# Performance work log

Measured on AMD Instinct MI355X. Metric: run time of the kernel, lower is better.

Reference implementation:

```python
import jax, jax.numpy as jnp
import numpy as np

# ---- MMAL-Net canonical configuration (baked constants of the module) ----
STRIDE = 32          # backbone stride: feature cell -> input pixels
FM = 14              # feature-map side (448 / 32)
RATIOS = [[4, 4], [3, 5], [5, 3],
          [6, 6], [5, 7], [7, 5],
          [8, 8], [6, 10], [10, 6], [7, 9], [9, 7]]
GROUP_SLICES = [(0, 3), (3, 6), (6, 11)]   # 3 scale groups of ratios
N_LIST = [3, 2, 1]                          # proposals kept per group
IOU_THRESHS = [0.25, 0.25, 0.25]


def _make_coords():
    # pixel-space [x0, y0, x1, y1] per sliding window, row-major (i outer, j inner)
    # matching the row-major flatten of the pooled feature maps.
    c = []
    for rh, rw in RATIOS:
        for i in range(FM - rh + 1):
            for j in range(FM - rw + 1):
                c.append([j * STRIDE, i * STRIDE,
                          (j + rw) * STRIDE - 1, (i + rh) * STRIDE - 1])
    return jnp.asarray(np.array(c, np.float32))

COORDS = _make_coords()                                   # [837, 4]
WIN_NUMS = [(FM - rh + 1) * (FM - rw + 1) for rh, rw in RATIOS]
GROUP_WINS = [sum(WIN_NUMS[a:b]) for a, b in GROUP_SLICES]  # [361, 241, 235]
GROUP_OFFSETS = [0, GROUP_WINS[0], GROUP_WINS[0] + GROUP_WINS[1]]
TOTAL_WINS = sum(GROUP_WINS)                              # 837


def _window_scores(x):
    """sum_c avgpool(x, r) == avgpool(sum_c x, r) -- fuse the channel reduction
    first so we avoid materializing [B, C, h', w'] per ratio."""
    y = jnp.sum(x, axis=1)  # [B, H, W]
    parts = []
    for rh, rw in RATIOS:
        s = jax.lax.reduce_window(y, jnp.float32(0), jax.lax.add,
                                  (1, rh, rw), (1, 1, 1), 'VALID') / (rh * rw)
        parts.append(s.reshape(y.shape[0], -1))
    return jnp.concatenate(parts, axis=1)  # [B, TOTAL_WINS]


def _nms_group(scores, coords, n_sel, iou_thresh):
    """Greedy NMS on one scale group: fixed n_sel iterations of
    (argmax over surviving windows, suppress IoU > thresh). If candidates run
    out, the last selected index is repeated (matches the torch fallback)."""
    W = scores.shape[0]
    area = (coords[:, 2] - coords[:, 0] + 1.) * (coords[:, 3] - coords[:, 1] + 1.)

    def step(carry, _):
        valid, last = carry
        any_v = jnp.any(valid)
        idx = jnp.argmax(jnp.where(valid, scores, -jnp.inf))
        idx = jnp.where(any_v, idx, last)
        sel = coords[idx]
        lt = jnp.maximum(coords[:, :2], sel[:2])
        rb = jnp.minimum(coords[:, 2:], sel[2:])
        wh = rb - lt + 1.
        inter = jnp.where((wh[:, 0] < 0) | (wh[:, 1] < 0), 0., wh[:, 0] * wh[:, 1])
        iou = inter / (area + area[idx] - inter)
        new_valid = (valid & (iou <= iou_thresh)).at[idx].set(False)
        new_valid = jnp.where(any_v, new_valid, valid)
        return (new_valid, idx), idx

    (_, _), sel = jax.lax.scan(step, (jnp.ones(W, bool), jnp.int32(0)),
                               None, length=n_sel)
    return sel  # [n_sel] int32 local indices


def setup_inputs() -> dict:
    key = jax.random.key(0)
    x = jax.random.normal(key, (64, 2048, FM, FM), dtype=jnp.float32)
    return {"x": x, "proposalN": 6}


def reference(x, proposalN):
    all_scores = _window_scores(x)  # [B, 837]
    idx_parts = []
    for g in range(len(N_LIST)):
        off, W = GROUP_OFFSETS[g], GROUP_WINS[g]
        sc = all_scores[:, off:off + W]
        co = COORDS[off:off + W]
        sel = jax.vmap(lambda s: _nms_group(s, co, N_LIST[g], IOU_THRESHS[g]))(sc)
        idx_parts.append(sel + off)
    proposal_indices = jnp.concatenate(idx_parts, axis=1)  # [B, proposalN]
    proposal_scores = jnp.take_along_axis(all_scores, proposal_indices, axis=1)
    return proposal_indices, proposal_scores, all_scores
```

## Files before the change

### kernel.cpp

```cpp
#include <hip/hip_runtime.h>
#include <math.h>

#define B 64
#define C 2048
#define FMH 14
#define HW 196
#define HW4 49
#define CHUNKS 32
#define CPC (C / CHUNKS)
#define NWIN 837
#define KMAX 6

__device__ __constant__ int d_RH[11]   = {4, 3, 5, 6, 5, 7, 8, 6, 10, 7, 9};
__device__ __constant__ int d_RW[11]   = {4, 5, 3, 6, 7, 5, 8, 10, 6, 9, 7};
__device__ __constant__ int d_WOFF[12] = {0, 121, 241, 361, 442, 522, 602, 651, 696, 741, 789, 837};

__global__ __launch_bounds__(256) void sum_channels_kernel(const float4* __restrict__ x,
                                                           float4* __restrict__ partial) {
    const int chunk = blockIdx.x;
    const int b     = blockIdx.y;
    const int lane  = threadIdx.x & 63;
    const int wave  = threadIdx.x >> 6;

    float4 acc = make_float4(0.f, 0.f, 0.f, 0.f);
    if (lane < HW4) {
        const float4* base = x + (size_t)(b * C + chunk * CPC) * HW4 + lane;
        #pragma unroll 4
        for (int k = 0; k < CPC / 4; ++k) {
            float4 v = base[(size_t)(wave + 4 * k) * HW4];
            acc.x += v.x; acc.y += v.y; acc.z += v.z; acc.w += v.w;
        }
    }

    __shared__ float4 sh[256];
    sh[threadIdx.x] = acc;
    __syncthreads();

    if (threadIdx.x < 64 && lane < HW4) {
        float4 a0 = sh[lane], a1 = sh[64 + lane], a2 = sh[128 + lane], a3 = sh[192 + lane];
        float4 s;
        s.x = (a0.x + a1.x) + (a2.x + a3.x);
        s.y = (a0.y + a1.y) + (a2.y + a3.y);
        s.z = (a0.z + a1.z) + (a2.z + a3.z);
        s.w = (a0.w + a1.w) + (a2.w + a3.w);
        partial[(size_t)(b * CHUNKS + chunk) * HW4 + lane] = s;
    }
}

__device__ inline void decode_box(int w, float& x0, float& y0, float& x1, float& y1, float& area) {
    int r = 0;
    while (w >= d_WOFF[r + 1]) ++r;
    int local = w - d_WOFF[r];
    int rh = d_RH[r], rw = d_RW[r];
    int wc = FMH - rw + 1;
    int i = local / wc, j = local - i * wc;
    x0 = (float)(j * 32);
    y0 = (float)(i * 32);
    x1 = (float)((j + rw) * 32 - 1);
    y1 = (float)((i + rh) * 32 - 1);
    area = (float)(rw * 32) * (float)(rh * 32);
}

__global__ __launch_bounds__(256) void scores_nms_kernel(const float* __restrict__ partial,
                                                         float* __restrict__ out) {
    const int g   = blockIdx.x;
    const int b   = blockIdx.y;
    const int tid = threadIdx.x;

    __shared__ float S[15][16];
    __shared__ float sc[361];

    const int ii = tid / FMH, jj = tid % FMH;
    if (tid < HW) {
        const float* p = partial + (size_t)b * CHUNKS * HW + tid;
        float acc = 0.f;
        #pragma unroll
        for (int ch = 0; ch < CHUNKS; ++ch) acc += p[(size_t)ch * HW];
        S[ii + 1][jj + 1] = acc;
    }
    if (tid < 16) S[0][tid] = 0.f;
    if (tid < 15) S[tid][0] = 0.f;
    __syncthreads();

    #pragma unroll
    for (int s = 1; s < 14; s <<= 1) {
        float add = 0.f;
        if (tid < HW && jj >= s) add = S[ii + 1][jj + 1 - s];
        __syncthreads();
        if (tid < HW) S[ii + 1][jj + 1] += add;
        __syncthreads();
    }
    #pragma unroll
    for (int s = 1; s < 14; s <<= 1) {
        float add = 0.f;
        if (tid < HW && ii >= s) add = S[ii + 1 - s][jj + 1];
        __syncthreads();
        if (tid < HW) S[ii + 1][jj + 1] += add;
        __syncthreads();
    }

    const int GOFFc[3] = {0, 361, 602};
    const int GWc[3]   = {361, 241, 235};
    const int NSELc[3] = {3, 2, 1};
    const int SLOTc[3] = {0, 3, 5};
    const int off = GOFFc[g], W = GWc[g];

    for (int wl = tid; wl < W; wl += 256) {
        int w = off + wl;
        int r = 0;
        while (w >= d_WOFF[r + 1]) ++r;
        int local = w - d_WOFF[r];
        int rh = d_RH[r], rw = d_RW[r];
        int wc = FMH - rw + 1;
        int i = local / wc, j = local - i * wc;
        float s = (S[i + rh][j + rw] - S[i][j + rw] - S[i + rh][j] + S[i][j]) / (float)(rh * rw);
        sc[wl] = s;
        out[768 + (size_t)b * NWIN + w] = s;
    }
    __syncthreads();

    if (tid >= 64) return;
    const int lane = tid;

    float sv[KMAX], bx0[KMAX], by0[KMAX], bx1[KMAX], by1[KMAX], bar[KMAX];
    unsigned vmask = 0;
    #pragma unroll
    for (int k = 0; k < KMAX; ++k) {
        int wl = lane + 64 * k;
        if (wl < W) {
            sv[k] = sc[wl];
            decode_box(off + wl, bx0[k], by0[k], bx1[k], by1[k], bar[k]);
            vmask |= (1u << k);
        } else {
            sv[k] = -INFINITY;
        }
    }

    int last = 0;
    const int nsel = NSELc[g];
    for (int it = 0; it < nsel; ++it) {
        float bv = -INFINITY; int bi = 0x7fffffff;
        #pragma unroll
        for (int k = 0; k < KMAX; ++k) {
            if (vmask & (1u << k)) {
                float v = sv[k];
                int wl = lane + 64 * k;
                if (v > bv || (v == bv && wl < bi)) { bv = v; bi = wl; }
            }
        }
        #pragma unroll
        for (int d = 1; d < 64; d <<= 1) {
            float ov = __shfl_xor(bv, d, 64);
            int   oi = __shfl_xor(bi, d, 64);
            if (ov > bv || (ov == bv && oi < bi)) { bv = ov; bi = oi; }
        }
        const bool any = (bv != -INFINITY);
        const int sel = any ? bi : last;
        last = sel;
        if (lane == 0) {
            out[(size_t)b * 6 + SLOTc[g] + it]       = (float)(off + sel);
            out[384 + (size_t)b * 6 + SLOTc[g] + it] = sc[sel];
        }
        if (any && it + 1 < nsel) {
            float sx0, sy0, sx1, sy1, sa;
            decode_box(off + sel, sx0, sy0, sx1, sy1, sa);
            #pragma unroll
            for (int k = 0; k < KMAX; ++k) {
                if (vmask & (1u << k)) {
                    float ltx = fmaxf(bx0[k], sx0), lty = fmaxf(by0[k], sy0);
                    float rbx = fminf(bx1[k], sx1), rby = fminf(by1[k], sy1);
                    float wx = rbx - ltx + 1.f, wy = rby - lty + 1.f;
                    float inter = (wx < 0.f || wy < 0.f) ? 0.f : wx * wy;
                    float iou = inter / (bar[k] + sa - inter);
                    if (iou > 0.25f) vmask &= ~(1u << k);
                }
            }
            if ((sel & 63) == lane) vmask &= ~(1u << (sel >> 6));
        }
        if (any && it + 1 >= nsel) {
            if ((sel & 63) == lane) vmask &= ~(1u << (sel >> 6));
        }
    }
}

extern "C" void kernel_launch(void* const* d_in, const int* in_sizes, int n_in,
                              void* d_out, int out_size, void* d_ws, size_t ws_size,
                              hipStream_t stream) {
    const float* x = (const float*)d_in[0];
    float* out = (float*)d_out;
    float* partial = (float*)d_ws;

    sum_channels_kernel<<<dim3(CHUNKS, B), 256, 0, stream>>>((const float4*)x, (float4*)partial);
    scores_nms_kernel<<<dim3(3, B), 256, 0, stream>>>(partial, out);
}
```

Measured before the change: 159.9 us.

## Fuse channel sum and NMS into one kernel via last-block atomic counter

Merges the channel-reduction kernel and the scores/NMS kernel into one launch. Each batch's blocks increment an atomic counter, and the last block to finish computes the integral image, all 837 window scores and NMS, with three waves handling the three groups in parallel. This removes the second kernel launch and its dependency gap, at the cost of a memset launch, extra fences and atomics, and serial tail work done by a single block per batch. The loop unroll is also increased to full.

```diff
diff --git a/kernel.cpp b/kernel.cpp
--- a/kernel.cpp
+++ b/kernel.cpp
@@ -14,38 +14,6 @@
 __device__ __constant__ int d_RH[11]   = {4, 3, 5, 6, 5, 7, 8, 6, 10, 7, 9};
 __device__ __constant__ int d_RW[11]   = {4, 5, 3, 6, 7, 5, 8, 10, 6, 9, 7};
 __device__ __constant__ int d_WOFF[12] = {0, 121, 241, 361, 442, 522, 602, 651, 696, 741, 789, 837};
-
-__global__ __launch_bounds__(256) void sum_channels_kernel(const float4* __restrict__ x,
-                                                           float4* __restrict__ partial) {
-    const int chunk = blockIdx.x;
-    const int b     = blockIdx.y;
-    const int lane  = threadIdx.x & 63;
-    const int wave  = threadIdx.x >> 6;
-
-    float4 acc = make_float4(0.f, 0.f, 0.f, 0.f);
-    if (lane < HW4) {
-        const float4* base = x + (size_t)(b * C + chunk * CPC) * HW4 + lane;
-        #pragma unroll 4
-        for (int k = 0; k < CPC / 4; ++k) {
-            float4 v = base[(size_t)(wave + 4 * k) * HW4];
-            acc.x += v.x; acc.y += v.y; acc.z += v.z; acc.w += v.w;
-        }
-    }
-
-    __shared__ float4 sh[256];
-    sh[threadIdx.x] = acc;
-    __syncthreads();
-
-    if (threadIdx.x < 64 && lane < HW4) {
-        float4 a0 = sh[lane], a1 = sh[64 + lane], a2 = sh[128 + lane], a3 = sh[192 + lane];
-        float4 s;
-        s.x = (a0.x + a1.x) + (a2.x + a3.x);
-        s.y = (a0.y + a1.y) + (a2.y + a3.y);
-        s.z = (a0.z + a1.z) + (a2.z + a3.z);
-        s.w = (a0.w + a1.w) + (a2.w + a3.w);
-        partial[(size_t)(b * CHUNKS + chunk) * HW4 + lane] = s;
-    }
-}
 
 __device__ inline void decode_box(int w, float& x0, float& y0, float& x1, float& y1, float& area) {
     int r = 0;
@@ -61,22 +29,62 @@
     area = (float)(rw * 32) * (float)(rh * 32);
 }
 
-__global__ __launch_bounds__(256) void scores_nms_kernel(const float* __restrict__ partial,
+__global__ __launch_bounds__(256) void appm_fused_kernel(const float4* __restrict__ x,
+                                                         float* __restrict__ partial,
+                                                         int* __restrict__ cnt,
                                                          float* __restrict__ out) {
-    const int g   = blockIdx.x;
-    const int b   = blockIdx.y;
-    const int tid = threadIdx.x;
+    const int chunk = blockIdx.x;
+    const int b     = blockIdx.y;
+    const int tid   = threadIdx.x;
+    const int lane  = tid & 63;
+    const int wave  = tid >> 6;
+
+    float4 acc = make_float4(0.f, 0.f, 0.f, 0.f);
+    if (lane < HW4) {
+        const float4* base = x + (size_t)(b * C + chunk * CPC) * HW4 + lane;
+        #pragma unroll
+        for (int k = 0; k < CPC / 4; ++k) {
+            float4 v = base[(size_t)(wave + 4 * k) * HW4];
+            acc.x += v.x; acc.y += v.y; acc.z += v.z; acc.w += v.w;
+        }
+    }
+
+    __shared__ float4 sh[256];
+    sh[tid] = acc;
+    __syncthreads();
+
+    if (tid < 64 && lane < HW4) {
+        float4 a0 = sh[lane], a1 = sh[64 + lane], a2 = sh[128 + lane], a3 = sh[192 + lane];
+        float4 s;
+        s.x = (a0.x + a1.x) + (a2.x + a3.x);
+        s.y = (a0.y + a1.y) + (a2.y + a3.y);
+        s.z = (a0.z + a1.z) + (a2.z + a3.z);
+        s.w = (a0.w + a1.w) + (a2.w + a3.w);
+        ((float4*)partial)[(size_t)(b * CHUNKS + chunk) * HW4 + lane] = s;
+    }
+
+    __syncthreads();
+    __threadfence();
+    __shared__ int s_last;
+    if (tid == 0) {
+        int old = __hip_atomic_fetch_add(&cnt[b], 1, __ATOMIC_ACQ_REL,
+                                         __HIP_MEMORY_SCOPE_AGENT);
+        s_last = (old == CHUNKS - 1) ? 1 : 0;
+    }
+    __syncthreads();
+    if (!s_last) return;
+    __threadfence();
 
     __shared__ float S[15][16];
-    __shared__ float sc[361];
+    __shared__ float sc[NWIN];
 
     const int ii = tid / FMH, jj = tid % FMH;
     if (tid < HW) {
         const float* p = partial + (size_t)b * CHUNKS * HW + tid;
-        float acc = 0.f;
-        #pragma unroll
-        for (int ch = 0; ch < CHUNKS; ++ch) acc += p[(size_t)ch * HW];
-        S[ii + 1][jj + 1] = acc;
+        float a = 0.f;
+        #pragma unroll
+        for (int ch = 0; ch < CHUNKS; ++ch) a += p[(size_t)ch * HW];
+        S[ii + 1][jj + 1] = a;
     }
     if (tid < 16) S[0][tid] = 0.f;
     if (tid < 15) S[tid][0] = 0.f;
@@ -99,14 +107,7 @@
         __syncthreads();
     }
 
-    const int GOFFc[3] = {0, 361, 602};
-    const int GWc[3]   = {361, 241, 235};
-    const int NSELc[3] = {3, 2, 1};
-    const int SLOTc[3] = {0, 3, 5};
-    const int off = GOFFc[g], W = GWc[g];
-
-    for (int wl = tid; wl < W; wl += 256) {
-        int w = off + wl;
+    for (int w = tid; w < NWIN; w += 256) {
         int r = 0;
         while (w >= d_WOFF[r + 1]) ++r;
         int local = w - d_WOFF[r];
@@ -114,13 +115,18 @@
         int wc = FMH - rw + 1;
         int i = local / wc, j = local - i * wc;
         float s = (S[i + rh][j + rw] - S[i][j + rw] - S[i + rh][j] + S[i][j]) / (float)(rh * rw);
-        sc[wl] = s;
+        sc[w] = s;
         out[768 + (size_t)b * NWIN + w] = s;
     }
     __syncthreads();
 
-    if (tid >= 64) return;
-    const int lane = tid;
+    const int g = wave;
+    if (g >= 3) return;
+    const int GOFFc[3] = {0, 361, 602};
+    const int GWc[3]   = {361, 241, 235};
+    const int NSELc[3] = {3, 2, 1};
+    const int SLOTc[3] = {0, 3, 5};
+    const int off = GOFFc[g], W = GWc[g];
 
     float sv[KMAX], bx0[KMAX], by0[KMAX], bx1[KMAX], by1[KMAX], bar[KMAX];
     unsigned vmask = 0;
@@ -128,7 +134,7 @@
     for (int k = 0; k < KMAX; ++k) {
         int wl = lane + 64 * k;
         if (wl < W) {
-            sv[k] = sc[wl];
+            sv[k] = sc[off + wl];
             decode_box(off + wl, bx0[k], by0[k], bx1[k], by1[k], bar[k]);
             vmask |= (1u << k);
         } else {
@@ -159,25 +165,24 @@
         last = sel;
         if (lane == 0) {
             out[(size_t)b * 6 + SLOTc[g] + it]       = (float)(off + sel);
-            out[384 + (size_t)b * 6 + SLOTc[g] + it] = sc[sel];
-        }
-        if (any && it + 1 < nsel) {
-            float sx0, sy0, sx1, sy1, sa;
-            decode_box(off + sel, sx0, sy0, sx1, sy1, sa);
-            #pragma unroll
-            for (int k = 0; k < KMAX; ++k) {
-                if (vmask & (1u << k)) {
-                    float ltx = fmaxf(bx0[k], sx0), lty = fmaxf(by0[k], sy0);
-                    float rbx = fminf(bx1[k], sx1), rby = fminf(by1[k], sy1);
-                    float wx = rbx - ltx + 1.f, wy = rby - lty + 1.f;
-                    float inter = (wx < 0.f || wy < 0.f) ? 0.f : wx * wy;
-                    float iou = inter / (bar[k] + sa - inter);
-                    if (iou > 0.25f) vmask &= ~(1u << k);
+            out[384 + (size_t)b * 6 + SLOTc[g] + it] = sc[off + sel];
+        }
+        if (any) {
+            if (it + 1 < nsel) {
+                float sx0, sy0, sx1, sy1, sa;
+                decode_box(off + sel, sx0, sy0, sx1, sy1, sa);
+                #pragma unroll
+                for (int k = 0; k < KMAX; ++k) {
+                    if (vmask & (1u << k)) {
+                        float ltx = fmaxf(bx0[k], sx0), lty = fmaxf(by0[k], sy0);
+                        float rbx = fminf(bx1[k], sx1), rby = fminf(by1[k], sy1);
+                        float wx = rbx - ltx + 1.f, wy = rby - lty + 1.f;
+                        float inter = (wx < 0.f || wy < 0.f) ? 0.f : wx * wy;
+                        float iou = inter / (bar[k] + sa - inter);
+                        if (iou > 0.25f) vmask &= ~(1u << k);
+                    }
                 }
             }
-            if ((sel & 63) == lane) vmask &= ~(1u << (sel >> 6));
-        }
-        if (any && it + 1 >= nsel) {
             if ((sel & 63) == lane) vmask &= ~(1u << (sel >> 6));
         }
     }
@@ -189,7 +194,8 @@
     const float* x = (const float*)d_in[0];
     float* out = (float*)d_out;
     float* partial = (float*)d_ws;
-
-    sum_channels_kernel<<<dim3(CHUNKS, B), 256, 0, stream>>>((const float4*)x, (float4*)partial);
-    scores_nms_kernel<<<dim3(3, B), 256, 0, stream>>>(partial, out);
+    int* cnt = (int*)((char*)d_ws + (size_t)B * CHUNKS * HW * sizeof(float));
+
+    hipMemsetAsync(cnt, 0, B * sizeof(int), stream);
+    appm_fused_kernel<<<dim3(CHUNKS, B), 256, 0, stream>>>((const float4*)x, partial, cnt, out);
 }
```

After: 557.9 us. +248.9%, slower.
